# Kernel tuning notes

Hardware: AMD Instinct MI355X
Metric: run time of the kernel (lower is better)

The kernel has to match this reference:

```python
import jax, jax.numpy as jnp
import numpy as np
from jax import lax

K = 16  # number of KNN neighbors (fixed in module)


def _knn_neighbors(x, k):
    # x: (B, 3, N) point coordinates -> neighbor coords (B, 3, N, K)
    inner = jnp.einsum('bdn,bdm->bnm', x, x)          # (B, N, N)
    sq = jnp.sum(x * x, axis=1)                        # (B, N)
    d2 = sq[:, :, None] + sq[:, None, :] - 2.0 * inner  # pairwise sq dists (B, N, N)
    _, nbr_idx = lax.top_k(-d2, k)                     # k nearest (incl. self), (B, N, K)
    # gather neighbor coordinates: expand x to (B, 3, 1, N), idx to (B, 1, N, K)
    neighbor = jnp.take_along_axis(x[:, :, None, :], nbr_idx[:, None, :, :], axis=3)
    return neighbor  # (B, 3, N, K)


def _down_index(neighbor, x, npts_ds):
    # center-diff saliency: sum of squared offsets to K neighbors per point
    diff = neighbor - x[:, :, :, None]                 # (B, 3, N, K)
    score = jnp.sum(diff * diff, axis=(1, 3))          # (B, N)
    _, idx = lax.top_k(score, npts_ds)                 # (B, npts_ds)
    return idx


def setup_inputs() -> dict:
    key = jax.random.key(0)
    k1, k2 = jax.random.split(key)
    B, N, C = 8, 4096, 128
    x = jax.random.normal(k1, (B, 3, N), dtype=jnp.float32)
    y = jax.random.normal(k2, (B, C, N), dtype=jnp.float32)
    return {"x": x, "y": y, "npts_ds": 2048}


def reference(x, y, npts_ds):
    B, _, N = x.shape
    C = y.shape[1]
    neighbor = _knn_neighbors(x, K)                    # ops.group(x, K, 'neighbor')
    idx = _down_index(neighbor, x, npts_ds)            # ops.down_index(...), (B, npts_ds)
    idx3 = jnp.broadcast_to(idx[:, None, :], (B, 3, npts_ds))
    idxC = jnp.broadcast_to(idx[:, None, :], (B, C, npts_ds))
    top_k_xyz = jnp.take_along_axis(x, idx3, axis=2)    # (B, 3, npts_ds)
    top_k_points = jnp.take_along_axis(y, idxC, axis=2)  # (B, C, npts_ds)
    return (top_k_xyz, top_k_points)
```

## Files before the change

### kernel.cpp

```cpp
#include <hip/hip_runtime.h>
#include <math.h>

#define BATCH 8
#define NPTS 4096
#define CHAN 128
#define KNN 16
#define SPLIT 4
#define CHUNK (NPTS / SPLIT)
#define ISPLIT 4
#define QCH (CHUNK / ISPLIT)
#define PTILE 64
#define EPC 24

typedef unsigned long long u64;

__device__ __forceinline__ u64 pack_key(float d2, int idx) {
  unsigned b = __float_as_uint(d2);
  b ^= (unsigned)((int)b >> 31) | 0x80000000u;
  return ((u64)b << 32) | (unsigned)idx;
}

__device__ __forceinline__ float d2_ref(float4 q, float ppx, float ppy,
                                        float ppz, float psq) {
  float inner = __fadd_rn(__fadd_rn(__fmul_rn(ppx, q.x), __fmul_rn(ppy, q.y)),
                          __fmul_rn(ppz, q.z));
  return __fsub_rn(__fadd_rn(psq, q.w), __fmul_rn(2.0f, inner));
}

__device__ __forceinline__ void ce_asc(u64& x, u64& y) {
  bool sw = y < x;
  u64 lo = sw ? y : x;
  u64 hi = sw ? x : y;
  x = lo;
  y = hi;
}

__device__ __forceinline__ void batcher_sort16_u64(u64 a[16]) {
#define CE(i, j) ce_asc(a[i], a[j])
  CE(0, 8); CE(1, 9); CE(2, 10); CE(3, 11);
  CE(4, 12); CE(5, 13); CE(6, 14); CE(7, 15);
  CE(0, 4); CE(1, 5); CE(2, 6); CE(3, 7);
  CE(8, 12); CE(9, 13); CE(10, 14); CE(11, 15);
  CE(4, 8); CE(5, 9); CE(6, 10); CE(7, 11);
  CE(0, 2); CE(1, 3); CE(4, 6); CE(5, 7);
  CE(8, 10); CE(9, 11); CE(12, 14); CE(13, 15);
  CE(2, 8); CE(3, 9); CE(6, 12); CE(7, 13);
  CE(2, 4); CE(3, 5); CE(6, 8); CE(7, 9); CE(10, 12); CE(11, 13);
  CE(0, 1); CE(2, 3); CE(4, 5); CE(6, 7);
  CE(8, 9); CE(10, 11); CE(12, 13); CE(14, 15);
  CE(1, 8); CE(3, 10); CE(5, 12); CE(7, 14);
  CE(1, 4); CE(3, 6); CE(5, 8); CE(7, 10); CE(9, 12); CE(11, 14);
  CE(1, 2); CE(3, 4); CE(5, 6); CE(7, 8); CE(9, 10); CE(11, 12); CE(13, 14);
#undef CE
}

__device__ __forceinline__ void bitonic_sort32(u64 a[32]) {
#pragma unroll
  for (int k = 2; k <= 32; k <<= 1) {
#pragma unroll
    for (int j = k >> 1; j > 0; j >>= 1) {
#pragma unroll
      for (int i = 0; i < 32; ++i) {
        int l = i ^ j;
        if (l > i) {
          if ((i & k) == 0) ce_asc(a[i], a[l]);
          else              ce_asc(a[l], a[i]);
        }
      }
    }
  }
}

__device__ __forceinline__ void merge_keep16(u64 T[16], const u64 A[16]) {
  u64 nt[16];
#pragma unroll
  for (int i = 0; i < 16; ++i) {
    u64 a = A[15 - i];
    nt[i] = (a < T[i]) ? a : T[i];
  }
#pragma unroll
  for (int j = 8; j > 0; j >>= 1) {
#pragma unroll
    for (int i = 0; i < 16; ++i) {
      int l = i ^ j;
      if (l > i) ce_asc(nt[i], nt[l]);
    }
  }
#pragma unroll
  for (int i = 0; i < 16; ++i) T[i] = nt[i];
}

__device__ __forceinline__ void ce_i32(int& x, int& y) {
  int lo = (x < y) ? x : y;
  int hi = (x < y) ? y : x;
  x = lo;
  y = hi;
}

__device__ __forceinline__ void batcher_sort16_i32(int a[16]) {
#define CE(i, j) ce_i32(a[i], a[j])
  CE(0, 8); CE(1, 9); CE(2, 10); CE(3, 11);
  CE(4, 12); CE(5, 13); CE(6, 14); CE(7, 15);
  CE(0, 4); CE(1, 5); CE(2, 6); CE(3, 7);
  CE(8, 12); CE(9, 13); CE(10, 14); CE(11, 15);
  CE(4, 8); CE(5, 9); CE(6, 10); CE(7, 11);
  CE(0, 2); CE(1, 3); CE(4, 6); CE(5, 7);
  CE(8, 10); CE(9, 11); CE(12, 14); CE(13, 15);
  CE(2, 8); CE(3, 9); CE(6, 12); CE(7, 13);
  CE(2, 4); CE(3, 5); CE(6, 8); CE(7, 9); CE(10, 12); CE(11, 13);
  CE(0, 1); CE(2, 3); CE(4, 5); CE(6, 7);
  CE(8, 9); CE(10, 11); CE(12, 13); CE(14, 15);
  CE(1, 8); CE(3, 10); CE(5, 12); CE(7, 14);
  CE(1, 4); CE(3, 6); CE(5, 8); CE(7, 10); CE(9, 12); CE(11, 14);
  CE(1, 2); CE(3, 4); CE(5, 6); CE(7, 8); CE(9, 10); CE(11, 12); CE(13, 14);
#undef CE
}

__device__ __forceinline__ void merge_keep16_i32(int T[16], const int A[16]) {
  int nt[16];
#pragma unroll
  for (int i = 0; i < 16; ++i) {
    int a = A[15 - i];
    nt[i] = (a < T[i]) ? a : T[i];
  }
#pragma unroll
  for (int j = 8; j > 0; j >>= 1) {
#pragma unroll
    for (int i = 0; i < 16; ++i) {
      int l = i ^ j;
      if (l > i) ce_i32(nt[i], nt[l]);
    }
  }
#pragma unroll
  for (int i = 0; i < 16; ++i) T[i] = nt[i];
}

__global__ __launch_bounds__(256) void knn_partial_kernel(
    const float* __restrict__ x, u64* __restrict__ pkey) {
  const int s = blockIdx.x % SPLIT;
  const int ntile = (blockIdx.x / SPLIT) % (NPTS / PTILE);
  const int b = blockIdx.x / (SPLIT * (NPTS / PTILE));
  const int p = threadIdx.x & (PTILE - 1);
  const int q4 = threadIdx.x >> 6;
  __shared__ float4 xs[CHUNK];
  __shared__ u64 ubuf[1024];

  const float* xb = x + (size_t)b * 3 * NPTS;
  for (int i = threadIdx.x; i < CHUNK; i += 256) {
    int gm = s * CHUNK + i;
    float px = xb[gm];
    float py = xb[NPTS + gm];
    float pz = xb[2 * NPTS + gm];
    float sq = __fadd_rn(__fadd_rn(__fmul_rn(px, px), __fmul_rn(py, py)),
                         __fmul_rn(pz, pz));
    xs[i] = make_float4(px, py, pz, sq);
  }

  const int n = ntile * PTILE + p;
  float ppx = xb[n];
  float ppy = xb[NPTS + n];
  float ppz = xb[2 * NPTS + n];
  float psq = __fadd_rn(__fadd_rn(__fmul_rn(ppx, ppx), __fmul_rn(ppy, ppy)),
                        __fmul_rn(ppz, ppz));
  __syncthreads();

  const int cbase = q4 * QCH;

  int T[16];
#pragma unroll
  for (int i = 0; i < 16; ++i) T[i] = 0x7FFFFFFF;
  int r17 = 0x7FFFFFFF;

#pragma unroll 1
  for (int base = 0; base < QCH; base += 16) {
    int A[16];
#pragma unroll
    for (int t = 0; t < 16; ++t) {
      float4 q = xs[cbase + base + t];
      int bits = __float_as_int(d2_ref(q, ppx, ppy, ppz, psq));
      A[t] = (bits & 0xFFFFFF00) | (base + t);
    }
    batcher_sort16_i32(A);
    int u[16];
#pragma unroll
    for (int i = 0; i < 16; ++i) {
      int a = A[15 - i];
      u[i] = (T[i] < a) ? a : T[i];
    }
#pragma unroll
    for (int w = 8; w > 0; w >>= 1) {
#pragma unroll
      for (int i = 0; i < 16; ++i) {
        if (i < w) u[i] = (u[i] < u[i + w]) ? u[i] : u[i + w];
      }
    }
    r17 = (r17 < u[0]) ? r17 : u[0];
    merge_keep16_i32(T, A);
  }

  const int tau = T[15] & 0xFFFFFF00;
  const bool slow = ((r17 & 0xFFFFFF00) == tau);

  u64 K[16];
  if (!slow) {
#pragma unroll
    for (int j = 0; j < 16; ++j) {
      int loc = cbase + (T[j] & 255);
      float4 q = xs[loc];
      float d2 = d2_ref(q, ppx, ppy, ppz, psq);
      K[j] = pack_key(d2, s * CHUNK + loc);
    }
    batcher_sort16_u64(K);
  } else {
    unsigned char* myb =
        reinterpret_cast<unsigned char*>(ubuf) + (unsigned)threadIdx.x * EPC;
    int cnt = 0;
#pragma unroll 4
    for (int m = 0; m < QCH; ++m) {
      float4 q = xs[cbase + m];
      int tb = __float_as_int(d2_ref(q, ppx, ppy, ppz, psq)) & 0xFFFFFF00;
      if (tb <= tau) {
        myb[cnt < EPC - 1 ? cnt : EPC - 1] = (unsigned char)m;
        ++cnt;
      }
    }
    u64 KK[32];
#pragma unroll
    for (int j = 0; j < EPC; ++j) {
      int loc = cbase + myb[j];
      float4 q = xs[loc];
      float d2 = d2_ref(q, ppx, ppy, ppz, psq);
      u64 k = pack_key(d2, s * CHUNK + loc);
      KK[j] = (j < cnt) ? k : ~0ull;
    }
#pragma unroll
    for (int j = EPC; j < 32; ++j) KK[j] = ~0ull;
    bitonic_sort32(KK);
#pragma unroll
    for (int j = 0; j < 16; ++j) K[j] = KK[j];
  }

  __syncthreads();
  u64(*L)[PTILE] = reinterpret_cast<u64(*)[PTILE]>(ubuf);
#pragma unroll 1
  for (int r = 1; r <= 3; ++r) {
    if (q4 == r) {
#pragma unroll
      for (int j = 0; j < 16; ++j) L[j][p] = K[j];
    }
    __syncthreads();
    if (q4 == 0) {
      u64 A64[16];
#pragma unroll
      for (int j = 0; j < 16; ++j) A64[j] = L[j][p];
      merge_keep16(K, A64);
    }
    __syncthreads();
  }
  if (q4 == 0) {
    u64* pb = pkey + ((size_t)(b * SPLIT + s) * KNN) * NPTS + n;
#pragma unroll
    for (int j = 0; j < 16; ++j) pb[(size_t)j * NPTS] = K[j];
  }
}

__global__ __launch_bounds__(256) void merge_score_kernel(
    const float* __restrict__ x, const u64* __restrict__ pkey,
    float* __restrict__ score) {
  const int tile = blockIdx.x % (NPTS / 64);
  const int b = blockIdx.x / (NPTS / 64);
  const int g = threadIdx.x >> 2;
  const int s = threadIdx.x & 3;
  const int n = tile * 64 + g;

  u64 T[16];
  {
    const u64* pb = pkey + ((size_t)(b * SPLIT + s) * KNN) * NPTS + n;
#pragma unroll
    for (int j = 0; j < 16; ++j) T[j] = pb[(size_t)j * NPTS];
  }

  u64 A[16];
#pragma unroll
  for (int j = 0; j < 16; ++j)
    A[j] = (u64)__shfl_xor((long long)T[j], 1);
  merge_keep16(T, A);
#pragma unroll
  for (int j = 0; j < 16; ++j)
    A[j] = (u64)__shfl_xor((long long)T[j], 2);
  merge_keep16(T, A);

  const float* xb = x + (size_t)b * 3 * NPTS;
  float P = 0.0f;
  if (s < 3) {
    const float* xd = xb + (size_t)s * NPTS;
    const float pc = xd[n];
    float r[8];
#pragma unroll
    for (int j = 0; j < 8; ++j) {
      float c0 = xd[(int)(unsigned)T[j]];
      float c1 = xd[(int)(unsigned)T[j + 8]];
      float e0 = __fsub_rn(c0, pc);
      float e1 = __fsub_rn(c1, pc);
      r[j] = __fadd_rn(__fmul_rn(e0, e0), __fmul_rn(e1, e1));
    }
    float t0 = __fadd_rn(r[0], r[1]);
    float t1 = __fadd_rn(r[2], r[3]);
    float t2 = __fadd_rn(r[4], r[5]);
    float t3 = __fadd_rn(r[6], r[7]);
    P = __fadd_rn(__fadd_rn(t0, t1), __fadd_rn(t2, t3));
  }
  float Pa = __shfl_xor(P, 1);
  float Pb = __shfl_xor(P, 2);
  if (s == 0)
    score[(size_t)b * NPTS + n] = __fadd_rn(__fadd_rn(P, Pa), Pb);
}

__global__ __launch_bounds__(256) void rank_scatter_kernel(
    const float* __restrict__ score, int* __restrict__ sel, int npts) {
  const int tile = blockIdx.x % (NPTS / 128);
  const int b = blockIdx.x / (NPTS / 128);
  const int p = threadIdx.x & 127;
  const int h = threadIdx.x >> 7;
  __shared__ float4 sv[NPTS / 4];
  __shared__ int cpart[128];

  const float* sb = score + (size_t)b * NPTS;
  const float4* sb4 = reinterpret_cast<const float4*>(sb);
  for (int i = threadIdx.x; i < NPTS / 4; i += 256) sv[i] = sb4[i];

  const int n = tile * 128 + p;
  const float sn = sb[n];
  __syncthreads();

  int c = 0;
  const int v0 = h * (NPTS / 8);
#pragma unroll 4
  for (int v = v0; v < v0 + NPTS / 8; ++v) {
    float4 f = sv[v];
    int gm = 4 * v;
    c += (f.x > sn) || (f.x == sn && gm < n);
    c += (f.y > sn) || (f.y == sn && gm + 1 < n);
    c += (f.z > sn) || (f.z == sn && gm + 2 < n);
    c += (f.w > sn) || (f.w == sn && gm + 3 < n);
  }
  if (h == 1) cpart[p] = c;
  __syncthreads();
  if (h == 0) {
    c += cpart[p];
    if (c < npts) sel[(size_t)b * npts + c] = n;
  }
}

__global__ __launch_bounds__(256) void gather_kernel(
    const float* __restrict__ x, const float* __restrict__ y,
    const int* __restrict__ sel, float* __restrict__ out, int npts,
    int total0, int total) {
  int tid = blockIdx.x * blockDim.x + threadIdx.x;
  if (tid >= total) return;
  if (tid < total0) {
    int j = tid % npts;
    int rest = tid / npts;
    int d = rest % 3;
    int b = rest / 3;
    int src = sel[b * npts + j];
    out[tid] = x[((size_t)b * 3 + d) * NPTS + src];
  } else {
    int t = tid - total0;
    int j = t % npts;
    int rest = t / npts;
    int c = rest % CHAN;
    int b = rest / CHAN;
    int src = sel[b * npts + j];
    out[tid] = y[((size_t)b * CHAN + c) * NPTS + src];
  }
}

extern "C" void kernel_launch(void* const* d_in, const int* in_sizes, int n_in,
                              void* d_out, int out_size, void* d_ws,
                              size_t ws_size, hipStream_t stream) {
  const float* x = (const float*)d_in[0];
  const float* y = (const float*)d_in[1];
  float* out = (float*)d_out;

  const int npts = out_size / (BATCH * (3 + CHAN));

  char* w = (char*)d_ws;
  u64* pkey = (u64*)w;
  w += sizeof(u64) * (size_t)BATCH * SPLIT * KNN * NPTS;
  float* score = (float*)w;
  w += sizeof(float) * (size_t)BATCH * NPTS;
  int* sel = (int*)w;

  knn_partial_kernel<<<BATCH * (NPTS / PTILE) * SPLIT, 256, 0, stream>>>(
      x, pkey);
  merge_score_kernel<<<BATCH * (NPTS / 64), 256, 0, stream>>>(x, pkey, score);
  rank_scatter_kernel<<<BATCH * (NPTS / 128), 256, 0, stream>>>(score, sel,
                                                                npts);
  const int total0 = BATCH * 3 * npts;
  gather_kernel<<<(out_size + 255) / 256, 256, 0, stream>>>(
      x, y, sel, out, npts, total0, out_size);
}
```

Baseline: 257.6 us.

## Precompute packed xyz+norm once and read candidates via uniform global loads

Adds a small pack kernel that writes each point as a float4 (x, y, z, squared norm) to workspace once. The KNN partial kernel drops its LDS staging and barrier and reads candidate points straight from global memory. The candidate base is made wave-uniform with readfirstlane so these loads can become scalar or broadcast loads. Ternary compares become min/max intrinsics. The cost is an extra kernel launch and reliance on cache hits instead of shared memory for the inner loop.

New measurement: 254.9 us. About the same (-1.0%).

```diff
diff --git a/kernel.cpp b/kernel.cpp
--- a/kernel.cpp
+++ b/kernel.cpp
@@ -91,8 +91,8 @@
 }
 
 __device__ __forceinline__ void ce_i32(int& x, int& y) {
-  int lo = (x < y) ? x : y;
-  int hi = (x < y) ? y : x;
+  int lo = min(x, y);
+  int hi = max(x, y);
   x = lo;
   y = hi;
 }
@@ -119,10 +119,7 @@
 __device__ __forceinline__ void merge_keep16_i32(int T[16], const int A[16]) {
   int nt[16];
 #pragma unroll
-  for (int i = 0; i < 16; ++i) {
-    int a = A[15 - i];
-    nt[i] = (a < T[i]) ? a : T[i];
-  }
+  for (int i = 0; i < 16; ++i) nt[i] = min(A[15 - i], T[i]);
 #pragma unroll
   for (int j = 8; j > 0; j >>= 1) {
 #pragma unroll
@@ -135,36 +132,36 @@
   for (int i = 0; i < 16; ++i) T[i] = nt[i];
 }
 
+__global__ __launch_bounds__(256) void pack_kernel(
+    const float* __restrict__ x, float4* __restrict__ packed) {
+  int t = blockIdx.x * 256 + threadIdx.x;
+  int b = t / NPTS;
+  int m = t % NPTS;
+  const float* xb = x + (size_t)b * 3 * NPTS;
+  float px = xb[m];
+  float py = xb[NPTS + m];
+  float pz = xb[2 * NPTS + m];
+  float sq = __fadd_rn(__fadd_rn(__fmul_rn(px, px), __fmul_rn(py, py)),
+                       __fmul_rn(pz, pz));
+  packed[t] = make_float4(px, py, pz, sq);
+}
+
 __global__ __launch_bounds__(256) void knn_partial_kernel(
-    const float* __restrict__ x, u64* __restrict__ pkey) {
+    const float4* __restrict__ packed, u64* __restrict__ pkey) {
   const int s = blockIdx.x % SPLIT;
   const int ntile = (blockIdx.x / SPLIT) % (NPTS / PTILE);
   const int b = blockIdx.x / (SPLIT * (NPTS / PTILE));
   const int p = threadIdx.x & (PTILE - 1);
   const int q4 = threadIdx.x >> 6;
-  __shared__ float4 xs[CHUNK];
   __shared__ u64 ubuf[1024];
 
-  const float* xb = x + (size_t)b * 3 * NPTS;
-  for (int i = threadIdx.x; i < CHUNK; i += 256) {
-    int gm = s * CHUNK + i;
-    float px = xb[gm];
-    float py = xb[NPTS + gm];
-    float pz = xb[2 * NPTS + gm];
-    float sq = __fadd_rn(__fadd_rn(__fmul_rn(px, px), __fmul_rn(py, py)),
-                         __fmul_rn(pz, pz));
-    xs[i] = make_float4(px, py, pz, sq);
-  }
-
+  const float4* pb4 = packed + (size_t)b * NPTS;
   const int n = ntile * PTILE + p;
-  float ppx = xb[n];
-  float ppy = xb[NPTS + n];
-  float ppz = xb[2 * NPTS + n];
-  float psq = __fadd_rn(__fadd_rn(__fmul_rn(ppx, ppx), __fmul_rn(ppy, ppy)),
-                        __fmul_rn(ppz, ppz));
-  __syncthreads();
-
-  const int cbase = q4 * QCH;
+  float4 pp = pb4[n];
+  const float ppx = pp.x, ppy = pp.y, ppz = pp.z, psq = pp.w;
+
+  const int cbase = __builtin_amdgcn_readfirstlane(s * CHUNK + q4 * QCH);
+  const float4* win = pb4 + cbase;
 
   int T[16];
 #pragma unroll
@@ -176,25 +173,22 @@
     int A[16];
 #pragma unroll
     for (int t = 0; t < 16; ++t) {
-      float4 q = xs[cbase + base + t];
+      float4 q = win[base + t];
       int bits = __float_as_int(d2_ref(q, ppx, ppy, ppz, psq));
       A[t] = (bits & 0xFFFFFF00) | (base + t);
     }
     batcher_sort16_i32(A);
     int u[16];
 #pragma unroll
-    for (int i = 0; i < 16; ++i) {
-      int a = A[15 - i];
-      u[i] = (T[i] < a) ? a : T[i];
-    }
+    for (int i = 0; i < 16; ++i) u[i] = max(T[i], A[15 - i]);
 #pragma unroll
     for (int w = 8; w > 0; w >>= 1) {
 #pragma unroll
       for (int i = 0; i < 16; ++i) {
-        if (i < w) u[i] = (u[i] < u[i + w]) ? u[i] : u[i + w];
+        if (i < w) u[i] = min(u[i], u[i + w]);
       }
     }
-    r17 = (r17 < u[0]) ? r17 : u[0];
+    r17 = min(r17, u[0]);
     merge_keep16_i32(T, A);
   }
 
@@ -205,10 +199,10 @@
   if (!slow) {
 #pragma unroll
     for (int j = 0; j < 16; ++j) {
-      int loc = cbase + (T[j] & 255);
-      float4 q = xs[loc];
+      int loc = T[j] & 255;
+      float4 q = win[loc];
       float d2 = d2_ref(q, ppx, ppy, ppz, psq);
-      K[j] = pack_key(d2, s * CHUNK + loc);
+      K[j] = pack_key(d2, cbase + loc);
     }
     batcher_sort16_u64(K);
   } else {
@@ -217,7 +211,7 @@
     int cnt = 0;
 #pragma unroll 4
     for (int m = 0; m < QCH; ++m) {
-      float4 q = xs[cbase + m];
+      float4 q = win[m];
       int tb = __float_as_int(d2_ref(q, ppx, ppy, ppz, psq)) & 0xFFFFFF00;
       if (tb <= tau) {
         myb[cnt < EPC - 1 ? cnt : EPC - 1] = (unsigned char)m;
@@ -227,10 +221,10 @@
     u64 KK[32];
 #pragma unroll
     for (int j = 0; j < EPC; ++j) {
-      int loc = cbase + myb[j];
-      float4 q = xs[loc];
+      int loc = myb[j];
+      float4 q = win[loc];
       float d2 = d2_ref(q, ppx, ppy, ppz, psq);
-      u64 k = pack_key(d2, s * CHUNK + loc);
+      u64 k = pack_key(d2, cbase + loc);
       KK[j] = (j < cnt) ? k : ~0ull;
     }
 #pragma unroll
@@ -386,14 +380,17 @@
   const int npts = out_size / (BATCH * (3 + CHAN));
 
   char* w = (char*)d_ws;
+  float4* packed = (float4*)w;
+  w += sizeof(float4) * (size_t)BATCH * NPTS;
   u64* pkey = (u64*)w;
   w += sizeof(u64) * (size_t)BATCH * SPLIT * KNN * NPTS;
   float* score = (float*)w;
   w += sizeof(float) * (size_t)BATCH * NPTS;
   int* sel = (int*)w;
 
+  pack_kernel<<<BATCH * NPTS / 256, 256, 0, stream>>>(x, packed);
   knn_partial_kernel<<<BATCH * (NPTS / PTILE) * SPLIT, 256, 0, stream>>>(
-      x, pkey);
+      packed, pkey);
   merge_score_kernel<<<BATCH * (NPTS / 64), 256, 0, stream>>>(x, pkey, score);
   rank_scatter_kernel<<<BATCH * (NPTS / 128), 256, 0, stream>>>(score, sel,
                                                                 npts);
```
